# Kernel optimization log

Hardware: AMD Instinct MI355X
Metric: run time of the kernel (lower is better)

Reference implementation:

```python
import jax, jax.numpy as jnp
import numpy as np

N, D, L, K = 128, 512, 512, 512


def setup_inputs() -> dict:
    key = jax.random.key(0)
    k1, k2 = jax.random.split(key, 2)
    x = jax.random.normal(k1, (N, D, L), dtype=jnp.float32)
    a = jnp.ones((D,), dtype=jnp.float32) * 0.5
    sigma = jax.random.uniform(k2, (D,), dtype=jnp.float32)
    return {"x": x, "a": a, "sigma": sigma}


def reference(x, a, sigma):
    # x: (N, D, L); a, sigma: (D,)
    Lf = x.shape[-1]
    n = jnp.arange(Lf, dtype=x.dtype)                      # (L,)
    k = jnp.arange(K, dtype=x.dtype)                       # (K,)
    denom = jnp.asarray(Lf - 1, dtype=x.dtype)
    # Hann-family window per feature: w[d,l] = a[d] - (1-a[d]) cos(2*pi*l/(L-1))
    window = a[:, None] - (1.0 - a)[:, None] * jnp.cos(n * (2.0 * jnp.pi) / denom)  # (D, L)
    # windowed + sigma-scaled signal (fused elementwise)
    xw = x * (window * jnp.exp(sigma / denom)[:, None])    # (N, D, L)
    # complex DFT basis exp(j*2*pi*l*k/(L-1)) split into real/imag GEMMs
    ang = (2.0 * jnp.pi / denom) * (n[:, None] * k[None, :])  # (L, K)
    Xr = jnp.einsum('ndl,lk->ndk', xw, jnp.cos(ang))
    Xi = jnp.einsum('ndl,lk->ndk', xw, jnp.sin(ang))
    # abs_flag=True -> magnitude spectrum
    return jnp.sqrt(Xr * Xr + Xi * Xi)                     # (N, D, K)
```

## Files before the change

kernel.cpp:

```cpp
#include <hip/hip_runtime.h>
#include <hip/hip_bf16.h>
#include <math.h>

#define N_  128
#define D_  512
#define L_  512
#define K_  512
#define M_  (N_*D_)

typedef __bf16 bf16x8 __attribute__((ext_vector_type(8)));
typedef float  f32x4  __attribute__((ext_vector_type(4)));
typedef unsigned short ushort_t;

__global__ void basis_kernel(const float* __restrict__ a,
                             const float* __restrict__ sigma,
                             ushort_t* __restrict__ Bc,
                             ushort_t* __restrict__ Bs,
                             float* __restrict__ P,
                             float* __restrict__ Q,
                             float* __restrict__ C) {
    int idx = blockIdx.x * 256 + threadIdx.x;
    int r = idx >> 9;
    int c = idx & 511;
    unsigned m = (unsigned)(r * c) % 511u;
    const float w0 = 6.283185307179586f / 511.0f;
    float sn, cs;
    sincosf((float)m * w0, &sn, &cs);
    __hip_bfloat16 bc = __float2bfloat16(cs);
    __hip_bfloat16 bs = __float2bfloat16(sn);
    ushort_t uc, us;
    __builtin_memcpy(&uc, &bc, 2);
    __builtin_memcpy(&us, &bs, 2);
    Bc[idx] = uc;
    Bs[idx] = us;
    if (idx < 512) {
        float e = expf(sigma[idx] * (1.0f / 511.0f));
        P[idx] = a[idx] * e;
        Q[idx] = -(1.0f - a[idx]) * e;
        C[idx] = cosf((float)idx * w0);
    }
}

static __device__ __forceinline__ unsigned pack_bf16x2(float lo, float hi) {
    __hip_bfloat162 h = __float22bfloat162_rn(make_float2(lo, hi));
    unsigned u;
    __builtin_memcpy(&u, &h, 4);
    return u;
}

static __device__ __forceinline__ void load_lds_128(const void* g, void* l) {
    __builtin_amdgcn_global_load_lds(
        (const __attribute__((address_space(1))) unsigned int*)g,
        (__attribute__((address_space(3))) unsigned int*)l,
        16, 0, 0);
}

__global__ __launch_bounds__(256, 2)
void dft_gemm4(const float* __restrict__ x,
               const ushort_t* __restrict__ Bc,
               const ushort_t* __restrict__ Bs,
               const float* __restrict__ P,
               const float* __restrict__ Q,
               const float* __restrict__ C,
               float* __restrict__ out) {
    __shared__ ushort_t sA [2 * 128 * 32];
    __shared__ ushort_t sBc[2 * 128 * 32];
    __shared__ ushort_t sBs[2 * 128 * 32];

    const int bhw = blockIdx.x;
    const int wg  = (bhw & 7) * 256 + (bhw >> 3);
    const int ng  = wg & 3;
    const int mg  = wg >> 2;
    const int m0  = mg * 128;
    const int n0  = ng * 128;

    const int tid  = threadIdx.x;
    const int w    = tid >> 6;
    const int lane = tid & 63;

    const int ar0 = tid >> 2;
    const int ac  = tid & 3;
    const int ar1 = ar0 + 64;
    const int apc = ac ^ ((ar0 >> 1) & 3);
    const int d0  = m0 & (D_ - 1);

    const float p0 = P[d0 + ar0], q0 = Q[d0 + ar0];
    const float p1 = P[d0 + ar1], q1 = Q[d0 + ar1];

    const float* xr0 = x + (size_t)(m0 + ar0) * L_ + ac * 8;
    const float* xr1 = x + (size_t)(m0 + ar1) * L_ + ac * 8;
    const float* Cc  = C + ac * 8;

    ushort_t* aD0 = sA + ar0 * 32 + apc * 8;
    ushort_t* aD1 = sA + ar1 * 32 + apc * 8;

    const int br0 = tid >> 2;
    const int bq0 = (tid & 3) ^ ((br0 >> 1) & 3);
    const int br1 = (256 + tid) >> 2;
    const int bq1 = ((256 + tid) & 3) ^ ((br1 >> 1) & 3);

    const ushort_t* bcS0 = Bc + (size_t)(n0 + br0) * L_ + bq0 * 8;
    const ushort_t* bcS1 = Bc + (size_t)(n0 + br1) * L_ + bq1 * 8;
    const ushort_t* bsS0 = Bs + (size_t)(n0 + br0) * L_ + bq0 * 8;
    const ushort_t* bsS1 = Bs + (size_t)(n0 + br1) * L_ + bq1 * 8;

    const int wm = w >> 1, wn = w & 1;
    const int ml = lane & 15, quad = lane >> 4;

    int aOff[4], bOff[4];
#pragma unroll
    for (int mi = 0; mi < 4; ++mi) {
        int ar = wm * 64 + mi * 16 + ml;
        int pc = quad ^ ((ar >> 1) & 3);
        aOff[mi] = ar * 32 + pc * 8;
    }
#pragma unroll
    for (int ni = 0; ni < 4; ++ni) {
        int br = wn * 64 + ni * 16 + ml;
        int pc = quad ^ ((br >> 1) & 3);
        bOff[ni] = br * 32 + pc * 8;
    }

    f32x4 acc_c[4][4], acc_s[4][4];
    const f32x4 zero = {0.f, 0.f, 0.f, 0.f};
#pragma unroll
    for (int mi = 0; mi < 4; ++mi)
#pragma unroll
        for (int ni = 0; ni < 4; ++ni) { acc_c[mi][ni] = zero; acc_s[mi][ni] = zero; }

#define STAGE_B(buf, kk)                                                      \
    do {                                                                      \
        const int bo_ = (buf) * 4096;                                         \
        load_lds_128(bcS0 + (kk), sBc + bo_ + w * 512);                       \
        load_lds_128(bcS1 + (kk), sBc + bo_ + 2048 + w * 512);                \
        load_lds_128(bsS0 + (kk), sBs + bo_ + w * 512);                       \
        load_lds_128(bsS1 + (kk), sBs + bo_ + 2048 + w * 512);                \
    } while (0)

    auto writeA = [&](int buf, float4 v00, float4 v01, float4 v10, float4 v11,
                      float4 cv0, float4 cv1) {
        int bo = buf * 4096;
        float w0a = fmaf(q0, cv0.x, p0), w0b = fmaf(q0, cv0.y, p0);
        float w0c = fmaf(q0, cv0.z, p0), w0d = fmaf(q0, cv0.w, p0);
        float w0e = fmaf(q0, cv1.x, p0), w0f = fmaf(q0, cv1.y, p0);
        float w0g = fmaf(q0, cv1.z, p0), w0h = fmaf(q0, cv1.w, p0);
        int4 s0;
        s0.x = (int)pack_bf16x2(v00.x * w0a, v00.y * w0b);
        s0.y = (int)pack_bf16x2(v00.z * w0c, v00.w * w0d);
        s0.z = (int)pack_bf16x2(v01.x * w0e, v01.y * w0f);
        s0.w = (int)pack_bf16x2(v01.z * w0g, v01.w * w0h);
        *(int4*)(aD0 + bo) = s0;
        float w1a = fmaf(q1, cv0.x, p1), w1b = fmaf(q1, cv0.y, p1);
        float w1c = fmaf(q1, cv0.z, p1), w1d = fmaf(q1, cv0.w, p1);
        float w1e = fmaf(q1, cv1.x, p1), w1f = fmaf(q1, cv1.y, p1);
        float w1g = fmaf(q1, cv1.z, p1), w1h = fmaf(q1, cv1.w, p1);
        int4 s1;
        s1.x = (int)pack_bf16x2(v10.x * w1a, v10.y * w1b);
        s1.y = (int)pack_bf16x2(v10.z * w1c, v10.w * w1d);
        s1.z = (int)pack_bf16x2(v11.x * w1e, v11.y * w1f);
        s1.w = (int)pack_bf16x2(v11.z * w1g, v11.w * w1h);
        *(int4*)(aD1 + bo) = s1;
    };

    auto compute_tile = [&](int buf) {
        const int bo = buf * 4096;
        bf16x8 af[4], bcf[4], bsf[4];
#pragma unroll
        for (int mi = 0; mi < 4; ++mi)
            af[mi] = *(const bf16x8*)&sA[bo + aOff[mi]];
#pragma unroll
        for (int ni = 0; ni < 4; ++ni) {
            bcf[ni] = *(const bf16x8*)&sBc[bo + bOff[ni]];
            bsf[ni] = *(const bf16x8*)&sBs[bo + bOff[ni]];
        }
#pragma unroll
        for (int mi = 0; mi < 4; ++mi)
#pragma unroll
            for (int ni = 0; ni < 4; ++ni) {
                acc_c[mi][ni] = __builtin_amdgcn_mfma_f32_16x16x32_bf16(
                    af[mi], bcf[ni], acc_c[mi][ni], 0, 0, 0);
                acc_s[mi][ni] = __builtin_amdgcn_mfma_f32_16x16x32_bf16(
                    af[mi], bsf[ni], acc_s[mi][ni], 0, 0, 0);
            }
    };

    float4 a00 = *(const float4*)(xr0 + 0);
    float4 a01 = *(const float4*)(xr0 + 4);
    float4 a10 = *(const float4*)(xr1 + 0);
    float4 a11 = *(const float4*)(xr1 + 4);
    float4 cv0 = *(const float4*)(Cc + 0);
    float4 cv1 = *(const float4*)(Cc + 4);
    STAGE_B(0, 0);
    writeA(0, a00, a01, a10, a11, cv0, cv1);
    __syncthreads();

    int cur = 0;
    for (int kk = 32; kk < L_; kk += 32) {
        a00 = *(const float4*)(xr0 + kk);
        a01 = *(const float4*)(xr0 + kk + 4);
        a10 = *(const float4*)(xr1 + kk);
        a11 = *(const float4*)(xr1 + kk + 4);
        cv0 = *(const float4*)(Cc + kk);
        cv1 = *(const float4*)(Cc + kk + 4);
        STAGE_B(cur ^ 1, kk);
        compute_tile(cur);
        writeA(cur ^ 1, a00, a01, a10, a11, cv0, cv1);
        __syncthreads();
        cur ^= 1;
    }
    compute_tile(cur);

#undef STAGE_B

#pragma unroll
    for (int mi = 0; mi < 4; ++mi)
#pragma unroll
        for (int ni = 0; ni < 4; ++ni) {
#pragma unroll
            for (int r = 0; r < 4; ++r) {
                float cv = acc_c[mi][ni][r];
                float sv = acc_s[mi][ni][r];
                int row = m0 + wm * 64 + mi * 16 + quad * 4 + r;
                int col = n0 + wn * 64 + ni * 16 + ml;
                out[(size_t)row * K_ + col] = sqrtf(cv * cv + sv * sv);
            }
        }
}

extern "C" void kernel_launch(void* const* d_in, const int* in_sizes, int n_in,
                              void* d_out, int out_size, void* d_ws, size_t ws_size,
                              hipStream_t stream) {
    (void)in_sizes; (void)n_in; (void)out_size; (void)ws_size;
    const float* x     = (const float*)d_in[0];
    const float* a     = (const float*)d_in[1];
    const float* sigma = (const float*)d_in[2];
    float* out = (float*)d_out;

    ushort_t* Bc = (ushort_t*)d_ws;
    ushort_t* Bs = Bc + 512 * 512;
    float*    P  = (float*)(Bs + 512 * 512);
    float*    Q  = P + 512;
    float*    C  = Q + 512;

    basis_kernel<<<dim3(1024), dim3(256), 0, stream>>>(a, sigma, Bc, Bs, P, Q, C);
    dft_gemm4<<<dim3(2048), dim3(256), 0, stream>>>(x, Bc, Bs, P, Q, C, out);
}
```

Before: 331.3 us.

## Exploit DFT conjugate symmetry to halve GEMM work with interleaved cos/sin basis

The basis has period 511, so for real input |X(k)| equals |X(511-k)|. The change builds a single basis of 256 frequencies, with cosine and sine rows interleaved, and runs one GEMM with one accumulator set. Adjacent lanes combine their squared cos/sin results with a shuffle, and the resulting magnitude is written to both k and 511-k. This roughly halves MFMA work and B-tile traffic, and the smaller LDS and register footprint allows a launch bound of 3 blocks per CU. The cost is output stores that are less coalesced, since odd lanes write mirrored columns.

```diff
diff --git a/kernel.cpp b/kernel.cpp
--- a/kernel.cpp
+++ b/kernel.cpp
@@ -6,6 +6,7 @@
 #define D_  512
 #define L_  512
 #define K_  512
+#define KH_ 256
 #define M_  (N_*D_)
 
 typedef __bf16 bf16x8 __attribute__((ext_vector_type(8)));
@@ -14,25 +15,23 @@
 
 __global__ void basis_kernel(const float* __restrict__ a,
                              const float* __restrict__ sigma,
-                             ushort_t* __restrict__ Bc,
-                             ushort_t* __restrict__ Bs,
+                             ushort_t* __restrict__ Bi,
                              float* __restrict__ P,
                              float* __restrict__ Q,
                              float* __restrict__ C) {
     int idx = blockIdx.x * 256 + threadIdx.x;
     int r = idx >> 9;
     int c = idx & 511;
-    unsigned m = (unsigned)(r * c) % 511u;
+    int k = r >> 1;
+    unsigned m = (unsigned)(k * c) % 511u;
     const float w0 = 6.283185307179586f / 511.0f;
     float sn, cs;
     sincosf((float)m * w0, &sn, &cs);
-    __hip_bfloat16 bc = __float2bfloat16(cs);
-    __hip_bfloat16 bs = __float2bfloat16(sn);
-    ushort_t uc, us;
-    __builtin_memcpy(&uc, &bc, 2);
-    __builtin_memcpy(&us, &bs, 2);
-    Bc[idx] = uc;
-    Bs[idx] = us;
+    float val = (r & 1) ? sn : cs;
+    __hip_bfloat16 bv = __float2bfloat16(val);
+    ushort_t uv;
+    __builtin_memcpy(&uv, &bv, 2);
+    Bi[idx] = uv;
     if (idx < 512) {
         float e = expf(sigma[idx] * (1.0f / 511.0f));
         P[idx] = a[idx] * e;
@@ -55,28 +54,28 @@
         16, 0, 0);
 }
 
-__global__ __launch_bounds__(256, 2)
-void dft_gemm4(const float* __restrict__ x,
-               const ushort_t* __restrict__ Bc,
-               const ushort_t* __restrict__ Bs,
+__global__ __launch_bounds__(256, 3)
+void dft_gemm9(const float* __restrict__ x,
+               const ushort_t* __restrict__ Bi,
                const float* __restrict__ P,
                const float* __restrict__ Q,
                const float* __restrict__ C,
                float* __restrict__ out) {
     __shared__ ushort_t sA [2 * 128 * 32];
-    __shared__ ushort_t sBc[2 * 128 * 32];
-    __shared__ ushort_t sBs[2 * 128 * 32];
-
-    const int bhw = blockIdx.x;
-    const int wg  = (bhw & 7) * 256 + (bhw >> 3);
-    const int ng  = wg & 3;
-    const int mg  = wg >> 2;
-    const int m0  = mg * 128;
-    const int n0  = ng * 128;
+    __shared__ ushort_t sBi[2 * 128 * 32];
+
+    const int b  = blockIdx.x;
+    const int wg = (b & 7) * 256 + (b >> 3);
+    const int ng = wg & 3;
+    const int mg = wg >> 2;
+    const int m0 = mg * 128;
+    const int n0 = ng * 128;
 
     const int tid  = threadIdx.x;
     const int w    = tid >> 6;
     const int lane = tid & 63;
+    const int ml   = lane & 15;
+    const int quad = lane >> 4;
 
     const int ar0 = tid >> 2;
     const int ac  = tid & 3;
@@ -94,18 +93,12 @@
     ushort_t* aD0 = sA + ar0 * 32 + apc * 8;
     ushort_t* aD1 = sA + ar1 * 32 + apc * 8;
 
-    const int br0 = tid >> 2;
-    const int bq0 = (tid & 3) ^ ((br0 >> 1) & 3);
-    const int br1 = (256 + tid) >> 2;
-    const int bq1 = ((256 + tid) & 3) ^ ((br1 >> 1) & 3);
-
-    const ushort_t* bcS0 = Bc + (size_t)(n0 + br0) * L_ + bq0 * 8;
-    const ushort_t* bcS1 = Bc + (size_t)(n0 + br1) * L_ + bq1 * 8;
-    const ushort_t* bsS0 = Bs + (size_t)(n0 + br0) * L_ + bq0 * 8;
-    const ushort_t* bsS1 = Bs + (size_t)(n0 + br1) * L_ + bq1 * 8;
+    const int brB = tid >> 2;
+    const int bqB = (tid & 3) ^ ((brB >> 1) & 3);
+    const ushort_t* biS0 = Bi + (size_t)(n0 + brB) * L_ + bqB * 8;
+    const ushort_t* biS1 = Bi + (size_t)(n0 + 64 + brB) * L_ + bqB * 8;
 
     const int wm = w >> 1, wn = w & 1;
-    const int ml = lane & 15, quad = lane >> 4;
 
     int aOff[4], bOff[4];
 #pragma unroll
@@ -121,20 +114,18 @@
         bOff[ni] = br * 32 + pc * 8;
     }
 
-    f32x4 acc_c[4][4], acc_s[4][4];
+    f32x4 acc[4][4];
     const f32x4 zero = {0.f, 0.f, 0.f, 0.f};
 #pragma unroll
     for (int mi = 0; mi < 4; ++mi)
 #pragma unroll
-        for (int ni = 0; ni < 4; ++ni) { acc_c[mi][ni] = zero; acc_s[mi][ni] = zero; }
+        for (int ni = 0; ni < 4; ++ni) acc[mi][ni] = zero;
 
 #define STAGE_B(buf, kk)                                                      \
     do {                                                                      \
         const int bo_ = (buf) * 4096;                                         \
-        load_lds_128(bcS0 + (kk), sBc + bo_ + w * 512);                       \
-        load_lds_128(bcS1 + (kk), sBc + bo_ + 2048 + w * 512);                \
-        load_lds_128(bsS0 + (kk), sBs + bo_ + w * 512);                       \
-        load_lds_128(bsS1 + (kk), sBs + bo_ + 2048 + w * 512);                \
+        load_lds_128(biS0 + (kk), sBi + bo_ + w * 512);                       \
+        load_lds_128(biS1 + (kk), sBi + bo_ + 2048 + w * 512);                \
     } while (0)
 
     auto writeA = [&](int buf, float4 v00, float4 v01, float4 v10, float4 v11,
@@ -164,24 +155,19 @@
 
     auto compute_tile = [&](int buf) {
         const int bo = buf * 4096;
-        bf16x8 af[4], bcf[4], bsf[4];
+        bf16x8 af[4], bf[4];
 #pragma unroll
         for (int mi = 0; mi < 4; ++mi)
             af[mi] = *(const bf16x8*)&sA[bo + aOff[mi]];
 #pragma unroll
-        for (int ni = 0; ni < 4; ++ni) {
-            bcf[ni] = *(const bf16x8*)&sBc[bo + bOff[ni]];
-            bsf[ni] = *(const bf16x8*)&sBs[bo + bOff[ni]];
-        }
+        for (int ni = 0; ni < 4; ++ni)
+            bf[ni] = *(const bf16x8*)&sBi[bo + bOff[ni]];
 #pragma unroll
         for (int mi = 0; mi < 4; ++mi)
 #pragma unroll
-            for (int ni = 0; ni < 4; ++ni) {
-                acc_c[mi][ni] = __builtin_amdgcn_mfma_f32_16x16x32_bf16(
-                    af[mi], bcf[ni], acc_c[mi][ni], 0, 0, 0);
-                acc_s[mi][ni] = __builtin_amdgcn_mfma_f32_16x16x32_bf16(
-                    af[mi], bsf[ni], acc_s[mi][ni], 0, 0, 0);
-            }
+            for (int ni = 0; ni < 4; ++ni)
+                acc[mi][ni] = __builtin_amdgcn_mfma_f32_16x16x32_bf16(
+                    af[mi], bf[ni], acc[mi][ni], 0, 0, 0);
     };
 
     float4 a00 = *(const float4*)(xr0 + 0);
@@ -218,11 +204,15 @@
         for (int ni = 0; ni < 4; ++ni) {
 #pragma unroll
             for (int r = 0; r < 4; ++r) {
-                float cv = acc_c[mi][ni][r];
-                float sv = acc_s[mi][ni][r];
-                int row = m0 + wm * 64 + mi * 16 + quad * 4 + r;
-                int col = n0 + wn * 64 + ni * 16 + ml;
-                out[(size_t)row * K_ + col] = sqrtf(cv * cv + sv * sv);
+                float v  = acc[mi][ni][r];
+                float sq = v * v;
+                sq += __shfl_xor(sq, 1);
+                float mag = sqrtf(sq);
+                int row  = m0 + wm * 64 + mi * 16 + quad * 4 + r;
+                int icol = n0 + wn * 64 + ni * 16 + ml;
+                int k    = icol >> 1;
+                int col  = (icol & 1) ? (K_ - 1 - k) : k;
+                out[(size_t)row * K_ + col] = mag;
             }
         }
 }
@@ -236,12 +226,11 @@
     const float* sigma = (const float*)d_in[2];
     float* out = (float*)d_out;
 
-    ushort_t* Bc = (ushort_t*)d_ws;
-    ushort_t* Bs = Bc + 512 * 512;
-    float*    P  = (float*)(Bs + 512 * 512);
+    ushort_t* Bi = (ushort_t*)d_ws;
+    float*    P  = (float*)(Bi + 512 * 512);
     float*    Q  = P + 512;
     float*    C  = Q + 512;
 
-    basis_kernel<<<dim3(1024), dim3(256), 0, stream>>>(a, sigma, Bc, Bs, P, Q, C);
-    dft_gemm4<<<dim3(2048), dim3(256), 0, stream>>>(x, Bc, Bs, P, Q, C, out);
-}
+    basis_kernel<<<dim3(1024), dim3(256), 0, stream>>>(a, sigma, Bi, P, Q, C);
+    dft_gemm9<<<dim3(2048), dim3(256), 0, stream>>>(x, Bi, P, Q, C, out);
+}
```

Result: faster. 294.0 us (-11.3%).
